# Performance work log

Measured on AMD Instinct MI355X. Metric: run time of the kernel, lower is better.

## Reference

```python
import jax, jax.numpy as jnp
import numpy as np
import math

B, T, D = 2, 2048, 4096
H, HD = 32, 128  # n_head, head_dim; H*HD == D
THETA = 10000.0


def _rope_tables(T, hd, theta):
    # standard RoPE: freqs_i = theta^(-2i/hd), angle[t,i] = t * freqs_i
    inv = 1.0 / (theta ** (np.arange(0, hd, 2, dtype=np.float32) / hd))  # [hd/2]
    ang = np.arange(T, dtype=np.float32)[:, None] * inv[None, :]          # [T, hd/2]
    return jnp.asarray(np.cos(ang)), jnp.asarray(np.sin(ang))


def setup_inputs() -> dict:
    key = jax.random.key(0)
    ks = jax.random.split(key, 5)
    scale = 1.0 / math.sqrt(D)
    x = jax.random.normal(ks[0], (B, T, D), dtype=jnp.float32)
    Wq = jax.random.normal(ks[1], (D, H * HD), dtype=jnp.float32) * scale
    Wk = jax.random.normal(ks[2], (D, H * HD), dtype=jnp.float32) * scale
    Wv = jax.random.normal(ks[3], (D, H * HD), dtype=jnp.float32) * scale
    Wo = jax.random.normal(ks[4], (D, D), dtype=jnp.float32) * scale
    fc, fs = _rope_tables(T, HD, THETA)
    return {"x": x, "freqs_cos": fc, "freqs_sin": fs,
            "Wq": Wq, "Wk": Wk, "Wv": Wv, "Wo": Wo}


def _apply_rope(t, cos, sin):
    # t: [B, T, H, HD]; complex rotation on interleaved (even, odd) pairs
    tp = t.reshape(*t.shape[:-1], HD // 2, 2)
    xr, xi = tp[..., 0], tp[..., 1]
    c = cos[None, :, None, :]  # [1, T, 1, HD/2]
    s = sin[None, :, None, :]
    out_r = xr * c - xi * s
    out_i = xr * s + xi * c
    return jnp.stack([out_r, out_i], axis=-1).reshape(t.shape)


def reference(x, freqs_cos, freqs_sin, Wq, Wk, Wv, Wo):
    Bc, Tc, _ = x.shape
    q = (x @ Wq).reshape(Bc, Tc, H, HD)
    k = (x @ Wk).reshape(Bc, Tc, H, HD)
    v = (x @ Wv).reshape(Bc, Tc, H, HD)
    q = _apply_rope(q, freqs_cos, freqs_sin)
    k = _apply_rope(k, freqs_cos, freqs_sin)
    scale = 1.0 / math.sqrt(HD)
    scores = jnp.einsum('bqhd,bkhd->bhqk', q, k) * scale  # [B,H,T,T]
    causal = jnp.tril(jnp.ones((Tc, Tc), dtype=bool))
    scores = jnp.where(causal[None, None], scores, -jnp.inf)
    attn = jax.nn.softmax(scores, axis=-1)
    y = jnp.einsum('bhqk,bkhd->bqhd', attn, v).reshape(Bc, Tc, H * HD)
    return y @ Wo
```

## Files before the change

### kernel.cpp

```cpp
#include <hip/hip_runtime.h>

typedef unsigned short ushort_t;
typedef unsigned int uint32;

typedef float f32x4 __attribute__((ext_vector_type(4)));
typedef __bf16 bf16x8 __attribute__((ext_vector_type(8)));
typedef unsigned short us8 __attribute__((ext_vector_type(8)));
typedef unsigned short us4 __attribute__((ext_vector_type(4)));

#define TSEQ 2048
#define DMODEL 4096

__device__ __forceinline__ ushort_t f2bf(float f) {
  uint32 u = __builtin_bit_cast(uint32, f);
  u += 0x7FFFu + ((u >> 16) & 1u);
  return (ushort_t)(u >> 16);
}
__device__ __forceinline__ float bf2f(ushort_t u) {
  return __builtin_bit_cast(float, ((uint32)u) << 16);
}

__device__ __forceinline__ void gload_lds16(const void* g, void* l) {
  auto gp = (const __attribute__((address_space(1))) void*)g;
  auto lp = (__attribute__((address_space(3))) void*)l;
  __builtin_amdgcn_global_load_lds(gp, lp, 16, 0, 0);
}

__global__ __launch_bounds__(256) void k_cast_bf16(const float* __restrict__ in,
                                                   ushort_t* __restrict__ out, int n4) {
  int g = blockIdx.x * 256 + threadIdx.x;
  if (g >= n4) return;
  float4 v = *(const float4*)(in + (size_t)g * 4);
  us4 o; o[0] = f2bf(v.x); o[1] = f2bf(v.y); o[2] = f2bf(v.z); o[3] = f2bf(v.w);
  *(us4*)(out + (size_t)g * 4) = o;
}

__global__ __launch_bounds__(256) void k_transpose_cast4(const float* __restrict__ W0,
                                                         const float* __restrict__ W1,
                                                         const float* __restrict__ W2,
                                                         const float* __restrict__ W3,
                                                         ushort_t* __restrict__ WTbase) {
  __shared__ __align__(16) ushort_t ts[64 * 72];
  const float* Ws[4] = {W0, W1, W2, W3};
  const float* W = Ws[blockIdx.z];
  ushort_t* WT = WTbase + (size_t)blockIdx.z * DMODEL * DMODEL;
  const int tid = threadIdx.x;
  const int n0 = blockIdx.x * 64, k0 = blockIdx.y * 64;
  #pragma unroll
  for (int it = 0; it < 4; ++it) {
    int e = it * 256 + tid;
    int r = e >> 4, c4 = e & 15;
    float4 v = *(const float4*)(W + (size_t)(k0 + r) * DMODEL + n0 + c4 * 4);
    us4 o; o[0] = f2bf(v.x); o[1] = f2bf(v.y); o[2] = f2bf(v.z); o[3] = f2bf(v.w);
    *(us4*)&ts[r * 72 + c4 * 4] = o;
  }
  __syncthreads();
  #pragma unroll
  for (int it = 0; it < 4; ++it) {
    int e = it * 256 + tid;
    int r2 = e >> 4, c4 = e & 15;
    us4 o;
    #pragma unroll
    for (int j = 0; j < 4; ++j) o[j] = ts[(c4 * 4 + j) * 72 + r2];
    *(us4*)(WT + (size_t)(n0 + r2) * DMODEL + k0 + c4 * 4) = o;
  }
}

template <bool OUT_BF16, bool ROPE>
__global__ __launch_bounds__(512, 2)
void k_gemm256(const ushort_t* __restrict__ A, const ushort_t* __restrict__ Bt,
               void* __restrict__ Cv, int M, int N, int K,
               const float* __restrict__ fc, const float* __restrict__ fs) {
  __shared__ __align__(16) ushort_t As[2][256 * 64];
  __shared__ __align__(16) ushort_t Bs[2][256 * 64];
  const int tid = threadIdx.x;
  const int w = tid >> 6, l = tid & 63;
  const int wr = w >> 2, wc = w & 3;
  const int lg = l >> 4, lc = l & 15;

  const int nwg = gridDim.x;
  const int cpx = nwg >> 3;
  const int wg = (blockIdx.x & 7) * cpx + (blockIdx.x >> 3);
  const int nbn = N >> 8;
  const int bm = wg / nbn, bn = wg % nbn;

  const ushort_t* Ab = A + (size_t)(bm * 256) * K;
  const ushort_t* Bb = Bt + (size_t)(bn * 256) * K;

  int aS0[2], aS1[2], bS0[2], bS1[2];
  #pragma unroll
  for (int j = 0; j < 2; ++j) {
    aS0[j] = (w < 4) ? (2 * w + j) : (8 + 2 * w + j);
    aS1[j] = aS0[j] + 8;
    int i2 = 2 * w + j;
    bS0[j] = (i2 >> 2) * 8 + (i2 & 3);
    bS1[j] = bS0[j] + 4;
  }
  const int rowoff = l >> 3;
  const int swz = (l & 7) ^ rowoff;

  int offA[8][2], offB[4][2];
  #pragma unroll
  for (int m = 0; m < 8; ++m)
    #pragma unroll
    for (int kk = 0; kk < 2; ++kk)
      offA[m][kk] = (wr * 128 + m * 16 + lc) * 64 + (((kk * 4 + lg) ^ (lc & 7)) * 8);
  #pragma unroll
  for (int n = 0; n < 4; ++n)
    #pragma unroll
    for (int kk = 0; kk < 2; ++kk)
      offB[n][kk] = (wc * 64 + n * 16 + lc) * 64 + (((kk * 4 + lg) ^ (lc & 7)) * 8);

  f32x4 acc[8][4];
  #pragma unroll
  for (int m = 0; m < 8; ++m)
    #pragma unroll
    for (int n = 0; n < 4; ++n) acc[m][n] = (f32x4){0.f, 0.f, 0.f, 0.f};

  const int NT = K >> 6;
  auto stg = [&](const ushort_t* gb, ushort_t* lds, int s, int tl) {
    int k0 = ((tl < NT) ? tl : (NT - 1)) << 6;
    gload_lds16(gb + (size_t)(s * 8 + rowoff) * K + k0 + swz * 8, lds + s * 512);
  };

  stg(Ab, As[0], aS0[0], 0); stg(Ab, As[0], aS0[1], 0);
  stg(Bb, Bs[0], bS0[0], 0); stg(Bb, Bs[0], bS0[1], 0);
  stg(Bb, Bs[0], bS1[0], 0); stg(Bb, Bs[0], bS1[1], 0);
  stg(Ab, As[0], aS1[0], 0); stg(Ab, As[0], aS1[1], 0);
  stg(Ab, As[1], aS0[0], 1); stg(Ab, As[1], aS0[1], 1);
  stg(Bb, Bs[1], bS0[0], 1); stg(Bb, Bs[1], bS0[1], 1);
  stg(Bb, Bs[1], bS1[0], 1); stg(Bb, Bs[1], bS1[1], 1);
  asm volatile("s_waitcnt vmcnt(6)" ::: "memory");
  __builtin_amdgcn_s_barrier();

  auto pass = [&](const ushort_t* Ac, const ushort_t* Bc, ushort_t* AsOth,
                  ushort_t* AsCur, ushort_t* BsCur, int tA1, int tM) {
    bf16x8 af[4][2], b0r[2][2], b1r[2][2];
    #pragma unroll
    for (int i = 0; i < 4; ++i)
      #pragma unroll
      for (int kk = 0; kk < 2; ++kk)
        af[i][kk] = *(const bf16x8*)&Ac[offA[i][kk]];
    #pragma unroll
    for (int j2 = 0; j2 < 2; ++j2)
      #pragma unroll
      for (int kk = 0; kk < 2; ++kk)
        b0r[j2][kk] = *(const bf16x8*)&Bc[offB[j2][kk]];
    stg(Ab, AsOth, aS1[0], tA1); stg(Ab, AsOth, aS1[1], tA1);
    asm volatile("s_waitcnt lgkmcnt(8)" ::: "memory");
    __builtin_amdgcn_s_barrier();
    asm volatile("s_waitcnt lgkmcnt(0)" ::: "memory");
    __builtin_amdgcn_sched_barrier(0);
    __builtin_amdgcn_s_setprio(1);
    #pragma unroll
    for (int i = 0; i < 4; ++i)
      #pragma unroll
      for (int j2 = 0; j2 < 2; ++j2)
        #pragma unroll
        for (int kk = 0; kk < 2; ++kk)
          acc[i][j2] = __builtin_amdgcn_mfma_f32_16x16x32_bf16(af[i][kk], b0r[j2][kk], acc[i][j2], 0, 0, 0);
    __builtin_amdgcn_s_setprio(0);
    __builtin_amdgcn_s_barrier();

    #pragma unroll
    for (int j2 = 0; j2 < 2; ++j2)
      #pragma unroll
      for (int kk = 0; kk < 2; ++kk)
        b1r[j2][kk] = *(const bf16x8*)&Bc[offB[2 + j2][kk]];
    stg(Ab, AsCur, aS0[0], tM); stg(Ab, AsCur, aS0[1], tM);
    asm volatile("" ::: "memory");
    __builtin_amdgcn_s_barrier();
    asm volatile("s_waitcnt lgkmcnt(0)" ::: "memory");
    __builtin_amdgcn_sched_barrier(0);
    __builtin_amdgcn_s_setprio(1);
    #pragma unroll
    for (int i = 0; i < 4; ++i)
      #pragma unroll
      for (int j2 = 0; j2 < 2; ++j2)
        #pragma unroll
        for (int kk = 0; kk < 2; ++kk)
          acc[i][2 + j2] = __builtin_amdgcn_mfma_f32_16x16x32_bf16(af[i][kk], b1r[j2][kk], acc[i][2 + j2], 0, 0, 0);
    __builtin_amdgcn_s_setprio(0);
    __builtin_amdgcn_s_barrier();

    #pragma unroll
    for (int i = 0; i < 4; ++i)
      #pragma unroll
      for (int kk = 0; kk < 2; ++kk)
        af[i][kk] = *(const bf16x8*)&Ac[offA[4 + i][kk]];
    stg(Bb, BsCur, bS0[0], tM); stg(Bb, BsCur, bS0[1], tM);
    asm volatile("" ::: "memory");
    __builtin_amdgcn_s_barrier();
    asm volatile("s_waitcnt lgkmcnt(0)" ::: "memory");
    __builtin_amdgcn_sched_barrier(0);
    __builtin_amdgcn_s_setprio(1);
    #pragma unroll
    for (int i = 0; i < 4; ++i)
      #pragma unroll
      for (int j2 = 0; j2 < 2; ++j2)
        #pragma unroll
        for (int kk = 0; kk < 2; ++kk)
          acc[4 + i][2 + j2] = __builtin_amdgcn_mfma_f32_16x16x32_bf16(af[i][kk], b1r[j2][kk], acc[4 + i][2 + j2], 0, 0, 0);
    __builtin_amdgcn_s_setprio(0);
    __builtin_amdgcn_s_barrier();

    stg(Bb, BsCur, bS1[0], tM); stg(Bb, BsCur, bS1[1], tM);
    asm volatile("" ::: "memory");
    __builtin_amdgcn_s_barrier();
    __builtin_amdgcn_s_setprio(1);
    #pragma unroll
    for (int i = 0; i < 4; ++i)
      #pragma unroll
      for (int j2 = 0; j2 < 2; ++j2)
        #pragma unroll
        for (int kk = 0; kk < 2; ++kk)
          acc[4 + i][j2] = __builtin_amdgcn_mfma_f32_16x16x32_bf16(af[i][kk], b0r[j2][kk], acc[4 + i][j2], 0, 0, 0);
    __builtin_amdgcn_s_setprio(0);
    asm volatile("s_waitcnt vmcnt(6)" ::: "memory");
    __builtin_amdgcn_s_barrier();
  };

  for (int t2 = 0; t2 < NT; t2 += 2) {
    pass(As[0], Bs[0], As[1], As[0], Bs[0], t2 + 1, t2 + 2);
    pass(As[1], Bs[1], As[0], As[1], Bs[1], t2 + 2, t2 + 3);
  }

  #pragma unroll
  for (int m = 0; m < 8; ++m) {
    int row0 = bm * 256 + wr * 128 + m * 16 + lg * 4;
    #pragma unroll
    for (int n = 0; n < 4; ++n) {
      int col = bn * 256 + wc * 64 + n * 16 + lc;
      if (ROPE) {
        int i0 = (col & 127) >> 1;
        #pragma unroll
        for (int r = 0; r < 4; ++r) {
          int tt = (row0 + r) & (TSEQ - 1);
          float c = fc[tt * 64 + i0];
          float s = fs[tt * 64 + i0];
          float v = acc[m][n][r];
          float p = __shfl_xor(v, 1);
          float ov = (lc & 1) ? (p * s + v * c) : (v * c - p * s);
          ((ushort_t*)Cv)[(size_t)(row0 + r) * N + col] = f2bf(ov);
        }
      } else {
        #pragma unroll
        for (int r = 0; r < 4; ++r) {
          float v = acc[m][n][r];
          if (OUT_BF16) ((ushort_t*)Cv)[(size_t)(row0 + r) * N + col] = f2bf(v);
          else          ((float*)Cv)[(size_t)(row0 + r) * N + col] = v;
        }
      }
    }
  }
}

__global__ __launch_bounds__(512, 2)
void k_attn(const ushort_t* __restrict__ Q, const ushort_t* __restrict__ Kb,
            const ushort_t* __restrict__ Vt, ushort_t* __restrict__ Y) {
  __shared__ __align__(16) ushort_t Ks[2][64 * 128];
  __shared__ __align__(16) ushort_t Vs[2][128 * 64];
  __shared__ __align__(16) ushort_t Ps[8][16 * 64];
  const int id = blockIdx.x;
  const int xcd = id & 7, slot = id >> 3;
  const int bx = slot & 7, gHi = slot >> 3;
  const int g = gHi * 8 + xcd;
  const int h = g & 31, b = g >> 5;
  const int tid = threadIdx.x;
  const int w = tid >> 6, l = tid & 63;
  const int lg = l >> 4, lc = l & 15;
  const float scale = 0.08838834764831845f;
  const float THR = 8.0f;

  auto stageKV = [&](int kv0, int buf) {
    #pragma unroll
    for (int i = 0; i < 2; ++i) {
      int seg = w * 2 + i;
      {
        int row = seg * 4 + (l >> 4);
        int csrc = (l & 15) ^ (row & 7);
        gload_lds16(Kb + (size_t)(b * TSEQ + kv0 + row) * DMODEL + h * 128 + csrc * 8,
                    &Ks[buf][seg * 512]);
      }
      {
        int row = seg * 8 + (l >> 3);
        int csrc = (l & 7) ^ (l >> 3);
        gload_lds16(Vt + (size_t)(h * 128 + row) * DMODEL + b * TSEQ + kv0 + csrc * 8,
                    &Vs[buf][seg * 512]);
      }
    }
  };

  for (int qi = 0; qi < 2; ++qi) {
    const int qt = qi ? (15 - bx) : bx;
    const int q0 = qt * 128;
    const int wrow0 = q0 + w * 16;

    bf16x8 qf[4];
    {
      const ushort_t* qp = Q + (size_t)(b * TSEQ + wrow0 + lc) * DMODEL + h * 128;
      #pragma unroll
      for (int ks = 0; ks < 4; ++ks) qf[ks] = *(const bf16x8*)(qp + ks * 32 + lg * 8);
    }

    float m_r[4], lp[4];
    #pragma unroll
    for (int r = 0; r < 4; ++r) { m_r[r] = -1e30f; lp[r] = 0.f; }
    f32x4 o[8];
    #pragma unroll
    for (int t = 0; t < 8; ++t) o[t] = (f32x4){0.f, 0.f, 0.f, 0.f};

    const int nkv = (qt + 1) * 2;
    stageKV(0, 0);
    for (int kt = 0; kt < nkv; ++kt) {
      const int cur = kt & 1;
      const int kv0 = kt * 64;
      if (kt + 1 < nkv) {
        stageKV((kt + 1) * 64, cur ^ 1);
        asm volatile("s_waitcnt vmcnt(4)" ::: "memory");
      } else {
        asm volatile("s_waitcnt vmcnt(0)" ::: "memory");
      }
      __builtin_amdgcn_s_barrier();

      if (kv0 <= wrow0 + 15) {
        f32x4 s[4];
        __builtin_amdgcn_s_setprio(1);
        #pragma unroll
        for (int n = 0; n < 4; ++n) {
          s[n] = (f32x4){0.f, 0.f, 0.f, 0.f};
          #pragma unroll
          for (int ks = 0; ks < 4; ++ks) {
            int row = n * 16 + lc;
            bf16x8 kf = *(const bf16x8*)&Ks[cur][row * 128 + ((ks * 32 + lg * 8) ^ ((row & 7) * 8))];
            s[n] = __builtin_amdgcn_mfma_f32_16x16x32_bf16(qf[ks], kf, s[n], 0, 0, 0);
          }
        }
        __builtin_amdgcn_s_setprio(0);

        float sv[4][4];
        if (kv0 + 63 > wrow0) {
          #pragma unroll
          for (int n = 0; n < 4; ++n)
            #pragma unroll
            for (int r = 0; r < 4; ++r) {
              float x = s[n][r] * scale;
              int kvg = kv0 + n * 16 + lc;
              int qg = wrow0 + lg * 4 + r;
              sv[n][r] = (kvg > qg) ? -1e30f : x;
            }
        } else {
          #pragma unroll
          for (int n = 0; n < 4; ++n)
            #pragma unroll
            for (int r = 0; r < 4; ++r) sv[n][r] = s[n][r] * scale;
        }

        float pmax[4];
        #pragma unroll
        for (int r = 0; r < 4; ++r)
          pmax[r] = fmaxf(fmaxf(sv[0][r], sv[1][r]), fmaxf(sv[2][r], sv[3][r]));
        bool ok = (pmax[0] <= m_r[0] + THR) && (pmax[1] <= m_r[1] + THR) &&
                  (pmax[2] <= m_r[2] + THR) && (pmax[3] <= m_r[3] + THR);
        if (!__all(ok)) {
          #pragma unroll
          for (int r = 0; r < 4; ++r) {
            float mx = pmax[r];
            #pragma unroll
            for (int off = 1; off < 16; off <<= 1) mx = fmaxf(mx, __shfl_xor(mx, off, 16));
            float mn = fmaxf(m_r[r], mx);
            float al = __expf(m_r[r] - mn);
            m_r[r] = mn;
            lp[r] *= al;
            #pragma unroll
            for (int t = 0; t < 8; ++t) o[t][r] *= al;
          }
        }

        #pragma unroll
        for (int n = 0; n < 4; ++n)
          #pragma unroll
          for (int r = 0; r < 4; ++r) {
            float p = __expf(sv[n][r] - m_r[r]);
            lp[r] += p;
            int row = lg * 4 + r, col = n * 16 + lc;
            Ps[w][row * 64 + (col ^ (lg * 16))] = f2bf(p);
          }

        __builtin_amdgcn_s_setprio(1);
        #pragma unroll
        for (int kvs = 0; kvs < 2; ++kvs) {
          bf16x8 pa = *(const bf16x8*)&Ps[w][lc * 64 + ((kvs * 32 + lg * 8) ^ ((lc >> 2) * 16))];
          #pragma unroll
          for (int t = 0; t < 8; ++t) {
            int vrow = t * 16 + lc;
            bf16x8 vb = *(const bf16x8*)&Vs[cur][vrow * 64 + ((kvs * 32 + lg * 8) ^ ((vrow & 7) * 8))];
            o[t] = __builtin_amdgcn_mfma_f32_16x16x32_bf16(pa, vb, o[t], 0, 0, 0);
          }
        }
        __builtin_amdgcn_s_setprio(0);
      }
      asm volatile("" ::: "memory");
      __builtin_amdgcn_s_barrier();
    }

    float linv[4];
    #pragma unroll
    for (int r = 0; r < 4; ++r) {
      float ls = lp[r];
      #pragma unroll
      for (int off = 1; off < 16; off <<= 1) ls += __shfl_xor(ls, off, 16);
      linv[r] = 1.0f / ls;
    }

    #pragma unroll
    for (int t = 0; t < 8; ++t)
      #pragma unroll
      for (int r = 0; r < 4; ++r) {
        int row = wrow0 + lg * 4 + r;
        int col = h * 128 + t * 16 + lc;
        Y[(size_t)(b * TSEQ + row) * DMODEL + col] = f2bf(o[t][r] * linv[r]);
      }
  }
}

extern "C" void kernel_launch(void* const* d_in, const int* in_sizes, int n_in,
                              void* d_out, int out_size, void* d_ws, size_t ws_size,
                              hipStream_t stream) {
  const float* x  = (const float*)d_in[0];
  const float* fc = (const float*)d_in[1];
  const float* fs = (const float*)d_in[2];
  const float* Wq = (const float*)d_in[3];
  const float* Wk = (const float*)d_in[4];
  const float* Wv = (const float*)d_in[5];
  const float* Wo = (const float*)d_in[6];

  const size_t SZ = (size_t)4096 * 4096;
  ushort_t* xb  = (ushort_t*)d_ws;
  ushort_t* WqT = xb + SZ;
  ushort_t* WkT = WqT + SZ;
  ushort_t* WvT = WkT + SZ;
  ushort_t* WoT = WvT + SZ;
  ushort_t* qb  = WoT + SZ;
  ushort_t* kb  = qb + SZ;
  ushort_t* vT  = kb + SZ;
  ushort_t* yb  = vT + SZ;

  k_cast_bf16<<<16384, 256, 0, stream>>>(x, xb, 4194304);
  dim3 tg(64, 64, 4);
  k_transpose_cast4<<<tg, 256, 0, stream>>>(Wq, Wk, Wv, Wo, WqT);

  k_gemm256<true, true><<<256, 512, 0, stream>>>(xb, WqT, qb, 4096, 4096, 4096, fc, fs);
  k_gemm256<true, true><<<256, 512, 0, stream>>>(xb, WkT, kb, 4096, 4096, 4096, fc, fs);
  k_gemm256<true, false><<<256, 512, 0, stream>>>(WvT, xb, vT, 4096, 4096, 4096, nullptr, nullptr);

  k_attn<<<512, 512, 0, stream>>>(qb, kb, vT, yb);

  k_gemm256<false, false><<<256, 512, 0, stream>>>(yb, WoT, d_out, 4096, 4096, 4096, nullptr, nullptr);
}
```

Baseline: 859.4 us.

## Restructure GEMM K-loop prefetch and fuse Q and K projections into one GEMM

The GEMM main loop is rebuilt so that each k-tile's A and B fragments are loaded from LDS at the end of the previous pass. The next tile's global-to-LDS stages are issued right after each barrier, and the fragment offset tables are replaced by base offsets plus constant strides, which cuts register pressure. Separately, the Q and K projections now run as a single 4096x8192 GEMM with 512 workgroups. This relies on WqT and WkT sitting next to each other in the workspace, and attention reads the fused QK buffer with a row stride of 8192. The intent is to hide LDS read latency behind MFMA work and drop one launch plus its tail effect. The risk is tighter barrier and vmcnt choreography that could create hazards, and the RoPE epilogue must still index the K half correctly.

```diff
diff --git a/kernel.cpp b/kernel.cpp
--- a/kernel.cpp
+++ b/kernel.cpp
@@ -66,6 +66,25 @@
   }
 }
 
+#define MM16(AF, BF, MO, NO)                                                     \
+  _Pragma("unroll") for (int i_ = 0; i_ < 4; ++i_)                               \
+  _Pragma("unroll") for (int j_ = 0; j_ < 2; ++j_)                               \
+  _Pragma("unroll") for (int k_ = 0; k_ < 2; ++k_)                               \
+    acc[(MO) + i_][(NO) + j_] = __builtin_amdgcn_mfma_f32_16x16x32_bf16(         \
+        AF[i_][k_], BF[j_][k_], acc[(MO) + i_][(NO) + j_], 0, 0, 0);
+
+#define LDA(DST, BASE, MO)                                                       \
+  _Pragma("unroll") for (int i_ = 0; i_ < 4; ++i_) {                             \
+    DST[i_][0] = *(const bf16x8*)((BASE) + ofsA0 + ((MO) + i_) * 1024);          \
+    DST[i_][1] = *(const bf16x8*)((BASE) + ofsA1 + ((MO) + i_) * 1024);          \
+  }
+#define LDB(DST, BASE, NO)                                                       \
+  _Pragma("unroll") for (int j_ = 0; j_ < 2; ++j_) {                             \
+    DST[j_][0] = *(const bf16x8*)((BASE) + ofsB0 + ((NO) + j_) * 1024);          \
+    DST[j_][1] = *(const bf16x8*)((BASE) + ofsB1 + ((NO) + j_) * 1024);          \
+  }
+#define MEMBAR() asm volatile("" ::: "memory")
+
 template <bool OUT_BF16, bool ROPE>
 __global__ __launch_bounds__(512, 2)
 void k_gemm256(const ushort_t* __restrict__ A, const ushort_t* __restrict__ Bt,
@@ -99,17 +118,10 @@
   const int rowoff = l >> 3;
   const int swz = (l & 7) ^ rowoff;
 
-  int offA[8][2], offB[4][2];
-  #pragma unroll
-  for (int m = 0; m < 8; ++m)
-    #pragma unroll
-    for (int kk = 0; kk < 2; ++kk)
-      offA[m][kk] = (wr * 128 + m * 16 + lc) * 64 + (((kk * 4 + lg) ^ (lc & 7)) * 8);
-  #pragma unroll
-  for (int n = 0; n < 4; ++n)
-    #pragma unroll
-    for (int kk = 0; kk < 2; ++kk)
-      offB[n][kk] = (wc * 64 + n * 16 + lc) * 64 + (((kk * 4 + lg) ^ (lc & 7)) * 8);
+  const int ofsA0 = (wr * 128 + lc) * 64 + (((0 * 4 + lg) ^ (lc & 7)) * 8);
+  const int ofsA1 = (wr * 128 + lc) * 64 + (((1 * 4 + lg) ^ (lc & 7)) * 8);
+  const int ofsB0 = (wc * 64 + lc) * 64 + (((0 * 4 + lg) ^ (lc & 7)) * 8);
+  const int ofsB1 = (wc * 64 + lc) * 64 + (((1 * 4 + lg) ^ (lc & 7)) * 8);
 
   f32x4 acc[8][4];
   #pragma unroll
@@ -123,106 +135,55 @@
     gload_lds16(gb + (size_t)(s * 8 + rowoff) * K + k0 + swz * 8, lds + s * 512);
   };
 
+  bf16x8 aX[4][2], b0[2][2], b1[2][2];
+
   stg(Ab, As[0], aS0[0], 0); stg(Ab, As[0], aS0[1], 0);
+  stg(Ab, As[0], aS1[0], 0); stg(Ab, As[0], aS1[1], 0);
   stg(Bb, Bs[0], bS0[0], 0); stg(Bb, Bs[0], bS0[1], 0);
   stg(Bb, Bs[0], bS1[0], 0); stg(Bb, Bs[0], bS1[1], 0);
-  stg(Ab, As[0], aS1[0], 0); stg(Ab, As[0], aS1[1], 0);
   stg(Ab, As[1], aS0[0], 1); stg(Ab, As[1], aS0[1], 1);
+  stg(Ab, As[1], aS1[0], 1); stg(Ab, As[1], aS1[1], 1);
   stg(Bb, Bs[1], bS0[0], 1); stg(Bb, Bs[1], bS0[1], 1);
   stg(Bb, Bs[1], bS1[0], 1); stg(Bb, Bs[1], bS1[1], 1);
-  asm volatile("s_waitcnt vmcnt(6)" ::: "memory");
+  asm volatile("s_waitcnt vmcnt(8)" ::: "memory");
   __builtin_amdgcn_s_barrier();
-
-  auto pass = [&](const ushort_t* Ac, const ushort_t* Bc, ushort_t* AsOth,
-                  ushort_t* AsCur, ushort_t* BsCur, int tA1, int tM) {
-    bf16x8 af[4][2], b0r[2][2], b1r[2][2];
-    #pragma unroll
-    for (int i = 0; i < 4; ++i)
-      #pragma unroll
-      for (int kk = 0; kk < 2; ++kk)
-        af[i][kk] = *(const bf16x8*)&Ac[offA[i][kk]];
-    #pragma unroll
-    for (int j2 = 0; j2 < 2; ++j2)
-      #pragma unroll
-      for (int kk = 0; kk < 2; ++kk)
-        b0r[j2][kk] = *(const bf16x8*)&Bc[offB[j2][kk]];
-    stg(Ab, AsOth, aS1[0], tA1); stg(Ab, AsOth, aS1[1], tA1);
-    asm volatile("s_waitcnt lgkmcnt(8)" ::: "memory");
-    __builtin_amdgcn_s_barrier();
-    asm volatile("s_waitcnt lgkmcnt(0)" ::: "memory");
-    __builtin_amdgcn_sched_barrier(0);
+  MEMBAR();
+  LDA(aX, As[0], 0);
+  LDB(b0, Bs[0], 0);
+
+  auto pass = [&](ushort_t* Ac, ushort_t* Bc, const ushort_t* Ao, const ushort_t* Bo, int t) {
+    LDB(b1, Bc, 2);
     __builtin_amdgcn_s_setprio(1);
-    #pragma unroll
-    for (int i = 0; i < 4; ++i)
-      #pragma unroll
-      for (int j2 = 0; j2 < 2; ++j2)
-        #pragma unroll
-        for (int kk = 0; kk < 2; ++kk)
-          acc[i][j2] = __builtin_amdgcn_mfma_f32_16x16x32_bf16(af[i][kk], b0r[j2][kk], acc[i][j2], 0, 0, 0);
+    MM16(aX, b0, 0, 0);
     __builtin_amdgcn_s_setprio(0);
-    __builtin_amdgcn_s_barrier();
-
-    #pragma unroll
-    for (int j2 = 0; j2 < 2; ++j2)
-      #pragma unroll
-      for (int kk = 0; kk < 2; ++kk)
-        b1r[j2][kk] = *(const bf16x8*)&Bc[offB[2 + j2][kk]];
-    stg(Ab, AsCur, aS0[0], tM); stg(Ab, AsCur, aS0[1], tM);
-    asm volatile("" ::: "memory");
-    __builtin_amdgcn_s_barrier();
-    asm volatile("s_waitcnt lgkmcnt(0)" ::: "memory");
-    __builtin_amdgcn_sched_barrier(0);
+    MEMBAR(); __builtin_amdgcn_s_barrier(); MEMBAR();
+    stg(Ab, Ac, aS0[0], t + 2); stg(Ab, Ac, aS0[1], t + 2);
+    stg(Bb, Bc, bS0[0], t + 2); stg(Bb, Bc, bS0[1], t + 2);
     __builtin_amdgcn_s_setprio(1);
-    #pragma unroll
-    for (int i = 0; i < 4; ++i)
-      #pragma unroll
-      for (int j2 = 0; j2 < 2; ++j2)
-        #pragma unroll
-        for (int kk = 0; kk < 2; ++kk)
-          acc[i][2 + j2] = __builtin_amdgcn_mfma_f32_16x16x32_bf16(af[i][kk], b1r[j2][kk], acc[i][2 + j2], 0, 0, 0);
+    MM16(aX, b1, 0, 2);
     __builtin_amdgcn_s_setprio(0);
-    __builtin_amdgcn_s_barrier();
-
-    #pragma unroll
-    for (int i = 0; i < 4; ++i)
-      #pragma unroll
-      for (int kk = 0; kk < 2; ++kk)
-        af[i][kk] = *(const bf16x8*)&Ac[offA[4 + i][kk]];
-    stg(Bb, BsCur, bS0[0], tM); stg(Bb, BsCur, bS0[1], tM);
-    asm volatile("" ::: "memory");
-    __builtin_amdgcn_s_barrier();
-    asm volatile("s_waitcnt lgkmcnt(0)" ::: "memory");
-    __builtin_amdgcn_sched_barrier(0);
+    LDA(aX, Ac, 4);
+    MEMBAR(); __builtin_amdgcn_s_barrier(); MEMBAR();
+    stg(Bb, Bc, bS1[0], t + 2); stg(Bb, Bc, bS1[1], t + 2);
     __builtin_amdgcn_s_setprio(1);
-    #pragma unroll
-    for (int i = 0; i < 4; ++i)
-      #pragma unroll
-      for (int j2 = 0; j2 < 2; ++j2)
-        #pragma unroll
-        for (int kk = 0; kk < 2; ++kk)
-          acc[4 + i][2 + j2] = __builtin_amdgcn_mfma_f32_16x16x32_bf16(af[i][kk], b1r[j2][kk], acc[4 + i][2 + j2], 0, 0, 0);
-    __builtin_amdgcn_s_setprio(0);
-    __builtin_amdgcn_s_barrier();
-
-    stg(Bb, BsCur, bS1[0], tM); stg(Bb, BsCur, bS1[1], tM);
-    asm volatile("" ::: "memory");
-    __builtin_amdgcn_s_barrier();
-    __builtin_amdgcn_s_setprio(1);
-    #pragma unroll
-    for (int i = 0; i < 4; ++i)
-      #pragma unroll
-      for (int j2 = 0; j2 < 2; ++j2)
-        #pragma unroll
-        for (int kk = 0; kk < 2; ++kk)
-          acc[4 + i][j2] = __builtin_amdgcn_mfma_f32_16x16x32_bf16(af[i][kk], b0r[j2][kk], acc[4 + i][j2], 0, 0, 0);
+    MM16(aX, b1, 4, 2);
     __builtin_amdgcn_s_setprio(0);
     asm volatile("s_waitcnt vmcnt(6)" ::: "memory");
-    __builtin_amdgcn_s_barrier();
+    MEMBAR(); __builtin_amdgcn_s_barrier(); MEMBAR();
+    stg(Ab, Ac, aS1[0], t + 2); stg(Ab, Ac, aS1[1], t + 2);
+    __builtin_amdgcn_s_setprio(1);
+    MM16(aX, b0, 4, 0);
+    __builtin_amdgcn_s_setprio(0);
+    if (t + 1 < NT) {
+      LDA(aX, Ao, 0);
+      LDB(b0, Bo, 0);
+    }
+    MEMBAR(); __builtin_amdgcn_s_barrier(); MEMBAR();
   };
 
-  for (int t2 = 0; t2 < NT; t2 += 2) {
-    pass(As[0], Bs[0], As[1], As[0], Bs[0], t2 + 1, t2 + 2);
-    pass(As[1], Bs[1], As[0], As[1], Bs[1], t2 + 2, t2 + 3);
+  for (int t = 0; t < NT; t += 2) {
+    pass(As[0], Bs[0], As[1], Bs[1], t);
+    pass(As[1], Bs[1], As[0], Bs[0], t + 1);
   }
 
   #pragma unroll
@@ -256,8 +217,8 @@
 }
 
 __global__ __launch_bounds__(512, 2)
-void k_attn(const ushort_t* __restrict__ Q, const ushort_t* __restrict__ Kb,
-            const ushort_t* __restrict__ Vt, ushort_t* __restrict__ Y) {
+void k_attn(const ushort_t* __restrict__ QK, const ushort_t* __restrict__ Vt,
+            ushort_t* __restrict__ Y) {
   __shared__ __align__(16) ushort_t Ks[2][64 * 128];
   __shared__ __align__(16) ushort_t Vs[2][128 * 64];
   __shared__ __align__(16) ushort_t Ps[8][16 * 64];
@@ -271,6 +232,7 @@
   const int lg = l >> 4, lc = l & 15;
   const float scale = 0.08838834764831845f;
   const float THR = 8.0f;
+  const int QKS = 8192;
 
   auto stageKV = [&](int kv0, int buf) {
     #pragma unroll
@@ -279,7 +241,7 @@
       {
         int row = seg * 4 + (l >> 4);
         int csrc = (l & 15) ^ (row & 7);
-        gload_lds16(Kb + (size_t)(b * TSEQ + kv0 + row) * DMODEL + h * 128 + csrc * 8,
+        gload_lds16(QK + (size_t)(b * TSEQ + kv0 + row) * QKS + 4096 + h * 128 + csrc * 8,
                     &Ks[buf][seg * 512]);
       }
       {
@@ -298,7 +260,7 @@
 
     bf16x8 qf[4];
     {
-      const ushort_t* qp = Q + (size_t)(b * TSEQ + wrow0 + lc) * DMODEL + h * 128;
+      const ushort_t* qp = QK + (size_t)(b * TSEQ + wrow0 + lc) * QKS + h * 128;
       #pragma unroll
       for (int ks = 0; ks < 4; ++ks) qf[ks] = *(const bf16x8*)(qp + ks * 32 + lg * 8);
     }
@@ -441,20 +403,18 @@
   ushort_t* WkT = WqT + SZ;
   ushort_t* WvT = WkT + SZ;
   ushort_t* WoT = WvT + SZ;
-  ushort_t* qb  = WoT + SZ;
-  ushort_t* kb  = qb + SZ;
-  ushort_t* vT  = kb + SZ;
+  ushort_t* qk  = WoT + SZ;
+  ushort_t* vT  = qk + 2 * SZ;
   ushort_t* yb  = vT + SZ;
 
   k_cast_bf16<<<16384, 256, 0, stream>>>(x, xb, 4194304);
   dim3 tg(64, 64, 4);
   k_transpose_cast4<<<tg, 256, 0, stream>>>(Wq, Wk, Wv, Wo, WqT);
 
-  k_gemm256<true, true><<<256, 512, 0, stream>>>(xb, WqT, qb, 4096, 4096, 4096, fc, fs);
-  k_gemm256<true, true><<<256, 512, 0, stream>>>(xb, WkT, kb, 4096, 4096, 4096, fc, fs);
+  k_gemm256<true, true><<<512, 512, 0, stream>>>(xb, WqT, qk, 4096, 8192, 4096, fc, fs);
   k_gemm256<true, false><<<256, 512, 0, stream>>>(WvT, xb, vT, 4096, 4096, 4096, nullptr, nullptr);
 
-  k_attn<<<512, 512, 0, stream>>>(qb, kb, vT, yb);
+  k_attn<<<512, 512, 0, stream>>>(qk, vT, yb);
 
   k_gemm256<false, false><<<256, 512, 0, stream>>>(yb, WoT, d_out, 4096, 4096, 4096, nullptr, nullptr);
 }
```

Measured after the change: 864.0 us. About the same (+0.5%).
